# Kernel optimization log

Measured on AMD Instinct MI355X. Metric: run time of the kernel, lower is better.

Reference implementation:

```python
import jax, jax.numpy as jnp
import numpy as np
from jax.ops import segment_sum

N_NODES = 100000
N_EDGES = 3200000
NUM_FEATURES = 256


def setup_inputs() -> dict:
    key = jax.random.key(0)
    ks = jax.random.split(key, 12)
    def lin(k, fan_in, fan_out):
        bound = 1.0 / np.sqrt(fan_in)
        kw, kb = jax.random.split(k)
        W = jax.random.uniform(kw, (fan_in, fan_out), jnp.float32, -bound, bound)
        b = jax.random.uniform(kb, (fan_out,), jnp.float32, -bound, bound)
        return W, b
    x = jax.random.normal(ks[0], (N_NODES, NUM_FEATURES), jnp.float32)
    edge_index = jax.random.randint(ks[1], (2, N_EDGES), 0, N_NODES, jnp.int64 if jax.config.jax_enable_x64 else jnp.int32)
    W1, b1 = lin(ks[2], NUM_FEATURES, 64)
    W2, b2 = lin(ks[3], 64, 32)
    W3, b3 = lin(ks[4], 32, 16)
    Ws02, bs02 = lin(ks[5], NUM_FEATURES, 32)
    Ws03, bs03 = lin(ks[6], NUM_FEATURES, 16)
    Ws13, bs13 = lin(ks[7], 64, 16)
    Wout, bout = lin(ks[8], 16, 1)
    return dict(x=x, edge_index=edge_index, W1=W1, b1=b1, W2=W2, b2=b2,
                W3=W3, b3=b3, Ws02=Ws02, bs02=bs02, Ws03=Ws03, bs03=bs03,
                Ws13=Ws13, bs13=bs13, Wout=Wout, bout=bout)


def _deg_inv_sqrt(edge_index, n_nodes):
    # gcn_norm with self-loops: degree counted at target nodes, +1 for self-loop
    dst = edge_index[1]
    deg = segment_sum(jnp.ones(edge_index.shape[1], jnp.float32), dst, num_segments=n_nodes) + 1.0
    return jnp.where(deg > 0, jax.lax.rsqrt(deg), 0.0)


def _gcn_conv(x, W, b, edge_index, dinv):
    # PyG GCNConv: h = x W; out[i] = sum_{j->i} dinv[j]*dinv[i]*h[j] + dinv[i]^2*h[i] + b
    src, dst = edge_index[0], edge_index[1]
    h = x @ W                                   # [N, out]
    norm = (dinv[src] * dinv[dst])[:, None]     # [E, 1]
    agg = segment_sum(h[src] * norm, dst, num_segments=x.shape[0])
    agg = agg + (dinv * dinv)[:, None] * h      # self-loop term
    return agg + b


def reference(x, edge_index, W1, b1, W2, b2, W3, b3,
              Ws02, bs02, Ws03, bs03, Ws13, bs13, Wout, bout):
    # Dropout in eval mode (identity).
    dinv = _deg_inv_sqrt(edge_index, x.shape[0])
    x1 = jax.nn.relu(_gcn_conv(x, W1, b1, edge_index, dinv))
    x2 = jax.nn.relu(_gcn_conv(x1, W2, b2, edge_index, dinv) + x @ Ws02 + bs02)
    x3 = jax.nn.relu(_gcn_conv(x2, W3, b3, edge_index, dinv)
                     + x @ Ws03 + bs03 + x1 @ Ws13 + bs13)
    return jax.nn.sigmoid(x3 @ Wout + bout)
```

## Files before the change

### kernel.cpp

```cpp
#include <hip/hip_runtime.h>
#include <hip/hip_bf16.h>
#include <math.h>


#define NBUCK_MAX 512
#define P1_CHUNK 8192
#define EPT 32
#define BCAP 9216

typedef __attribute__((ext_vector_type(8))) short bfrag;
typedef __attribute__((ext_vector_type(4))) float f4_t;

__device__ inline float uaf(unsigned u) { return __uint_as_float(u); }
__device__ inline ushort f2bf(float f) {
    __hip_bfloat16 b = __float2bfloat16(f);
    return *reinterpret_cast<ushort*>(&b);
}
__device__ inline bfrag cvt8(const float4 a, const float4 b) {
    union { ushort u[8]; bfrag f; } r;
    r.u[0] = f2bf(a.x); r.u[1] = f2bf(a.y); r.u[2] = f2bf(a.z); r.u[3] = f2bf(a.w);
    r.u[4] = f2bf(b.x); r.u[5] = f2bf(b.y); r.u[6] = f2bf(b.z); r.u[7] = f2bf(b.w);
    return r.f;
}
__device__ inline bfrag ld_bfrag(const ushort* p) {
    const uint4 raw = *reinterpret_cast<const uint4*>(p);
    return *reinterpret_cast<const bfrag*>(&raw);
}


__global__ __launch_bounds__(256) void bucket_hist_kernel(
    const int* __restrict__ dst, int E, int* __restrict__ bucket_count, int nbuckets)
{
    __shared__ int lhist[NBUCK_MAX];
    for (int i = threadIdx.x; i < nbuckets; i += 256) lhist[i] = 0;
    __syncthreads();
    const int stride = gridDim.x * 256;
    for (int e = blockIdx.x * 256 + threadIdx.x; e < E; e += stride)
        atomicAdd(&lhist[dst[e] >> 8], 1);
    __syncthreads();
    for (int i = threadIdx.x; i < nbuckets; i += 256) {
        int c = lhist[i];
        if (c) atomicAdd(&bucket_count[i], c);
    }
}

__global__ __launch_bounds__(512) void bucket_scan_kernel(
    const int* __restrict__ bucket_count, int* __restrict__ bucket_base,
    int* __restrict__ bucket_cursor, int nbuckets)
{
    __shared__ int tmp[512];
    const int tid = threadIdx.x;
    int v = (tid < nbuckets) ? bucket_count[tid] : 0;
    tmp[tid] = v;
    __syncthreads();
    for (int off = 1; off < 512; off <<= 1) {
        int t = (tid >= off) ? tmp[tid - off] : 0;
        __syncthreads();
        tmp[tid] += t;
        __syncthreads();
    }
    if (tid < nbuckets) {
        int base = tmp[tid] - v;
        bucket_base[tid]   = base;
        bucket_cursor[tid] = base;
    }
}

__global__ __launch_bounds__(256) void partition_kernel(
    const int* __restrict__ src, const int* __restrict__ dst, int E,
    int* __restrict__ bucket_cursor, unsigned int* __restrict__ keys, int nbuckets)
{
    __shared__ int hist[NBUCK_MAX];
    __shared__ int lofs[NBUCK_MAX];
    __shared__ int gbase[NBUCK_MAX];
    __shared__ int lcur[NBUCK_MAX];
    __shared__ int ssum[256];
    __shared__ unsigned int stage[P1_CHUNK];
    __shared__ int gidx[P1_CHUNK];

    const int tid = threadIdx.x;
    const int e0  = blockIdx.x * P1_CHUNK;
    const int nE  = min(P1_CHUNK, E - e0);

    for (int i = tid; i < NBUCK_MAX; i += 256) { hist[i] = 0; lcur[i] = 0; }
    __syncthreads();

    int myb[EPT];
    unsigned int mypk[EPT];
#pragma unroll
    for (int j = 0; j < EPT; ++j) {
        const int e = e0 + tid + j * 256;
        if (e < E) {
            const int d = dst[e];
            myb[j]  = d >> 8;
            mypk[j] = ((unsigned int)(d & 255) << 17) | (unsigned int)src[e];
            atomicAdd(&hist[myb[j]], 1);
        } else myb[j] = -1;
    }
    __syncthreads();

    int a0 = (2 * tid     < nbuckets) ? hist[2 * tid]     : 0;
    int a1 = (2 * tid + 1 < nbuckets) ? hist[2 * tid + 1] : 0;
    ssum[tid] = a0 + a1;
    __syncthreads();
    for (int off = 1; off < 256; off <<= 1) {
        int t = (tid >= off) ? ssum[tid - off] : 0;
        __syncthreads();
        ssum[tid] += t;
        __syncthreads();
    }
    const int ex = ssum[tid] - (a0 + a1);
    if (2 * tid     < nbuckets) lofs[2 * tid]     = ex;
    if (2 * tid + 1 < nbuckets) lofs[2 * tid + 1] = ex + a0;
    __syncthreads();

    for (int i = tid; i < nbuckets; i += 256)
        gbase[i] = atomicAdd(&bucket_cursor[i], hist[i]);
    __syncthreads();

#pragma unroll
    for (int j = 0; j < EPT; ++j) {
        if (myb[j] >= 0) {
            const int b = myb[j];
            const int l = lofs[b] + atomicAdd(&lcur[b], 1);
            stage[l] = mypk[j];
            gidx[l]  = gbase[b] - lofs[b] + l;
        }
    }
    __syncthreads();

    for (int i = tid; i < nE; i += 256)
        keys[gidx[i]] = stage[i];
}

__global__ __launch_bounds__(256) void csr_build_kernel(
    const unsigned int* __restrict__ keys, const int* __restrict__ bucket_base,
    const int* __restrict__ bucket_count,
    int* __restrict__ row_off, float* __restrict__ dinv, int* __restrict__ col,
    int N, int E)
{
    __shared__ unsigned int inb[BCAP];
    __shared__ int outv[BCAP];
    __shared__ int hist[256];
    __shared__ int lofs[256];
    __shared__ int ssum[256];

    const int tid  = threadIdx.x;
    const int b    = blockIdx.x;
    const int base = bucket_base[b];
    const int cnt  = min(bucket_count[b], BCAP);
    const int n0   = b << 8;
    const int nn   = min(256, N - n0);

    for (int i = tid; i < cnt; i += 256) inb[i] = keys[base + i];
    hist[tid] = 0;
    __syncthreads();

    for (int i = tid; i < cnt; i += 256)
        atomicAdd(&hist[inb[i] >> 17], 1);
    __syncthreads();

    ssum[tid] = hist[tid];
    __syncthreads();
    for (int off = 1; off < 256; off <<= 1) {
        int t = (tid >= off) ? ssum[tid - off] : 0;
        __syncthreads();
        ssum[tid] += t;
        __syncthreads();
    }
    lofs[tid] = ssum[tid] - hist[tid];

    if (tid < nn) {
        row_off[n0 + tid] = base + lofs[tid];
        dinv[n0 + tid]    = rsqrtf((float)hist[tid] + 1.0f);
    }
    if (b == 0 && tid == 0) row_off[N] = E;
    __syncthreads();

    hist[tid] = 0;
    __syncthreads();

    for (int i = tid; i < cnt; i += 256) {
        const unsigned int k = inb[i];
        const int node = k >> 17;
        const int l = lofs[node] + atomicAdd(&hist[node], 1);
        outv[l] = (int)(k & 0x1FFFF);
    }
    __syncthreads();

    for (int i = tid; i < cnt; i += 256)
        col[base + i] = outv[i];
}


__global__ __launch_bounds__(256) void prep_weights_kernel(
    const float* __restrict__ W1, const float* __restrict__ Ws02,
    const float* __restrict__ Ws03, const float* __restrict__ W2,
    const float* __restrict__ Ws13, const float* __restrict__ W3,
    ushort* __restrict__ Wt0, ushort* __restrict__ Wt1, ushort* __restrict__ Wt2)
{
    int idx = blockIdx.x * 256 + threadIdx.x;
    if (idx < 32768) {
        int f = idx >> 8, k = idx & 255;
        float v = 0.f;
        if (f < 64)       v = W1[k * 64 + f];
        else if (f < 96)  v = Ws02[k * 32 + (f - 64)];
        else if (f < 112) v = Ws03[k * 16 + (f - 96)];
        Wt0[idx] = f2bf(v);
    } else if (idx < 32768 + 3072) {
        int t = idx - 32768;
        int f = t >> 6, k = t & 63;
        float v = (f < 32) ? W2[k * 32 + f] : Ws13[k * 16 + (f - 32)];
        Wt1[t] = f2bf(v);
    } else if (idx < 32768 + 3072 + 512) {
        int t = idx - 32768 - 3072;
        int f = t >> 5, k = t & 31;
        Wt2[t] = f2bf(W3[k * 16 + f]);
    }
}


__global__ __launch_bounds__(256, 4) void gemm_mfma0(
    const float* __restrict__ X, const ushort* __restrict__ Wt0,
    const float* __restrict__ bs02, const float* __restrict__ bs03,
    const float* __restrict__ dinv,
    __hip_bfloat16* __restrict__ g1, float* __restrict__ pre2,
    float* __restrict__ pre3, int N)
{
    const int tid  = threadIdx.x;
    const int lane = tid & 63;
    const int wf   = tid >> 6;
    const int n0   = blockIdx.x * 64;
    const int mrow = lane & 15;
    const int kq   = (lane >> 4) * 8;

    f4_t acc[4][2];
#pragma unroll
    for (int a = 0; a < 4; ++a)
#pragma unroll
        for (int b = 0; b < 2; ++b) acc[a][b] = {0.f, 0.f, 0.f, 0.f};

    const float* xrow[4];
#pragma unroll
    for (int mt = 0; mt < 4; ++mt) {
        int r = n0 + mt * 16 + mrow;
        r = (r < N) ? r : (N - 1);
        xrow[mt] = &X[(size_t)r * 256 + kq];
    }
    const ushort* wrow[2];
#pragma unroll
    for (int ft = 0; ft < 2; ++ft)
        wrow[ft] = &Wt0[(size_t)(wf * 32 + ft * 16 + mrow) * 256 + kq];

#pragma unroll
    for (int p = 0; p < 8; ++p) {
        bfrag bf[2];
#pragma unroll
        for (int ft = 0; ft < 2; ++ft)
            bf[ft] = ld_bfrag(&wrow[ft][p * 32]);
        bfrag af[4];
#pragma unroll
        for (int mt = 0; mt < 4; ++mt) {
            const float4 u0 = *reinterpret_cast<const float4*>(&xrow[mt][p * 32]);
            const float4 u1 = *reinterpret_cast<const float4*>(&xrow[mt][p * 32 + 4]);
            af[mt] = cvt8(u0, u1);
        }
#pragma unroll
        for (int mt = 0; mt < 4; ++mt)
#pragma unroll
            for (int ft = 0; ft < 2; ++ft)
                acc[mt][ft] = __builtin_amdgcn_mfma_f32_16x16x32_bf16(
                    af[mt], bf[ft], acc[mt][ft], 0, 0, 0);
    }

#pragma unroll
    for (int mt = 0; mt < 4; ++mt) {
#pragma unroll
        for (int ft = 0; ft < 2; ++ft) {
            const int fg = wf * 32 + ft * 16 + mrow;
#pragma unroll
            for (int r = 0; r < 4; ++r) {
                const int n = n0 + mt * 16 + (lane >> 4) * 4 + r;
                if (n >= N) continue;
                const float a = acc[mt][ft][r];
                if (fg < 64) {
                    g1[(size_t)n * 64 + fg] = __float2bfloat16(dinv[n] * a);
                } else if (fg < 96) {
                    pre2[(size_t)n * 32 + (fg - 64)] = a + bs02[fg - 64];
                } else if (fg < 112) {
                    pre3[(size_t)n * 16 + (fg - 96)] = a + bs03[fg - 96];
                }
            }
        }
    }
}

__global__ __launch_bounds__(256) void gemm_mfma1(
    const ushort* __restrict__ X1, const ushort* __restrict__ Wt1,
    const float* __restrict__ bs13, const float* __restrict__ dinv,
    __hip_bfloat16* __restrict__ g2, float* __restrict__ pre3, int N)
{
    const int tid  = threadIdx.x;
    const int lane = tid & 63;
    const int wave = tid >> 6;
    const int n0   = blockIdx.x * 128 + wave * 32;
    const int mrow = lane & 15;
    const int kq   = (lane >> 4) * 8;

    f4_t acc[2][3];
#pragma unroll
    for (int a = 0; a < 2; ++a)
#pragma unroll
        for (int b = 0; b < 3; ++b) acc[a][b] = {0.f, 0.f, 0.f, 0.f};

    const ushort* xrow[2];
#pragma unroll
    for (int mt = 0; mt < 2; ++mt) {
        int r = n0 + mt * 16 + mrow;
        r = (r < N) ? r : (N - 1);
        xrow[mt] = &X1[(size_t)r * 64 + kq];
    }
    const ushort* wrow[3];
#pragma unroll
    for (int ft = 0; ft < 3; ++ft)
        wrow[ft] = &Wt1[(size_t)(ft * 16 + mrow) * 64 + kq];

#pragma unroll
    for (int p = 0; p < 2; ++p) {
        bfrag af[2], bf[3];
#pragma unroll
        for (int mt = 0; mt < 2; ++mt) af[mt] = ld_bfrag(&xrow[mt][p * 32]);
#pragma unroll
        for (int ft = 0; ft < 3; ++ft) bf[ft] = ld_bfrag(&wrow[ft][p * 32]);
#pragma unroll
        for (int mt = 0; mt < 2; ++mt)
#pragma unroll
            for (int ft = 0; ft < 3; ++ft)
                acc[mt][ft] = __builtin_amdgcn_mfma_f32_16x16x32_bf16(
                    af[mt], bf[ft], acc[mt][ft], 0, 0, 0);
    }

#pragma unroll
    for (int mt = 0; mt < 2; ++mt) {
#pragma unroll
        for (int ft = 0; ft < 3; ++ft) {
            const int fg = ft * 16 + mrow;
#pragma unroll
            for (int r = 0; r < 4; ++r) {
                const int n = n0 + mt * 16 + (lane >> 4) * 4 + r;
                if (n >= N) continue;
                const float a = acc[mt][ft][r];
                if (fg < 32) {
                    g2[(size_t)n * 32 + fg] = __float2bfloat16(dinv[n] * a);
                } else {
                    pre3[(size_t)n * 16 + (fg - 32)] += a + bs13[fg - 32];
                }
            }
        }
    }
}

__global__ __launch_bounds__(256) void gemm_mfma2(
    const ushort* __restrict__ X2, const ushort* __restrict__ Wt2,
    const float* __restrict__ dinv, __hip_bfloat16* __restrict__ g3, int N)
{
    const int tid  = threadIdx.x;
    const int lane = tid & 63;
    const int wave = tid >> 6;
    const int n0   = blockIdx.x * 128 + wave * 32;
    const int mrow = lane & 15;
    const int kq   = (lane >> 4) * 8;

    f4_t acc[2];
#pragma unroll
    for (int a = 0; a < 2; ++a) acc[a] = {0.f, 0.f, 0.f, 0.f};

    const bfrag bf = ld_bfrag(&Wt2[(size_t)mrow * 32 + kq]);
#pragma unroll
    for (int mt = 0; mt < 2; ++mt) {
        int r = n0 + mt * 16 + mrow;
        r = (r < N) ? r : (N - 1);
        const bfrag af = ld_bfrag(&X2[(size_t)r * 32 + kq]);
        acc[mt] = __builtin_amdgcn_mfma_f32_16x16x32_bf16(af, bf, acc[mt], 0, 0, 0);
    }

#pragma unroll
    for (int mt = 0; mt < 2; ++mt) {
#pragma unroll
        for (int r = 0; r < 4; ++r) {
            const int n = n0 + mt * 16 + (lane >> 4) * 4 + r;
            if (n >= N) continue;
            g3[(size_t)n * 16 + mrow] = __float2bfloat16(dinv[n] * acc[mt][r]);
        }
    }
}


template<int F, int MODE>
__global__ __launch_bounds__(256) void agg_kernel(
    const ushort* __restrict__ g, const float* __restrict__ dinv,
    const int* __restrict__ row_off, const int* __restrict__ col,
    const float* __restrict__ bias, const float* __restrict__ pre,
    const float* __restrict__ Wout, const float* __restrict__ bout,
    void* __restrict__ out, int N)
{
    constexpr int FG  = F / 4;
    constexpr int EPW = 64 / FG;
    constexpr int U   = (F == 64) ? 8 : (F == 32 ? 4 : 2);

    const int lane = threadIdx.x & 63;
    const int wv   = threadIdx.x >> 6;
    const int i    = blockIdx.x * 4 + wv;
    if (i >= N) return;

    const int fg = lane % FG;
    const int eo = lane / FG;
    const int fb = fg * 4;

    float a0 = 0.f, a1 = 0.f, a2 = 0.f, a3 = 0.f;
    const int s = row_off[i], e = row_off[i + 1];
    int p = s + eo;
    for (; p + (U - 1) * EPW < e; p += U * EPW) {
        int js[U];
#pragma unroll
        for (int u = 0; u < U; ++u) js[u] = col[p + u * EPW];
        uint2 w[U];
#pragma unroll
        for (int u = 0; u < U; ++u)
            w[u] = *reinterpret_cast<const uint2*>(&g[(size_t)js[u] * F + fb]);
#pragma unroll
        for (int u = 0; u < U; ++u) {
            a0 += uaf(w[u].x << 16);
            a1 += uaf(w[u].x & 0xffff0000u);
            a2 += uaf(w[u].y << 16);
            a3 += uaf(w[u].y & 0xffff0000u);
        }
    }
    for (; p < e; p += EPW) {
        const uint2 w0 = *reinterpret_cast<const uint2*>(&g[(size_t)col[p] * F + fb]);
        a0 += uaf(w0.x << 16);
        a1 += uaf(w0.x & 0xffff0000u);
        a2 += uaf(w0.y << 16);
        a3 += uaf(w0.y & 0xffff0000u);
    }
#pragma unroll
    for (int off = FG; off < 64; off <<= 1) {
        a0 += __shfl_xor(a0, off);
        a1 += __shfl_xor(a1, off);
        a2 += __shfl_xor(a2, off);
        a3 += __shfl_xor(a3, off);
    }

    const uint2 ws = *reinterpret_cast<const uint2*>(&g[(size_t)i * F + fb]);
    const float di = dinv[i];
    float v0 = di * (a0 + uaf(ws.x << 16))         + bias[fb + 0];
    float v1 = di * (a1 + uaf(ws.x & 0xffff0000u)) + bias[fb + 1];
    float v2 = di * (a2 + uaf(ws.y << 16))         + bias[fb + 2];
    float v3 = di * (a3 + uaf(ws.y & 0xffff0000u)) + bias[fb + 3];
    if (MODE != 0) {
        const float4 pv = *reinterpret_cast<const float4*>(&pre[(size_t)i * F + fb]);
        v0 += pv.x; v1 += pv.y; v2 += pv.z; v3 += pv.w;
    }
    v0 = fmaxf(v0, 0.f); v1 = fmaxf(v1, 0.f);
    v2 = fmaxf(v2, 0.f); v3 = fmaxf(v3, 0.f);

    if (MODE != 2) {
        if (lane < FG) {
            uint2 o;
            o.x = (unsigned)f2bf(v0) | ((unsigned)f2bf(v1) << 16);
            o.y = (unsigned)f2bf(v2) | ((unsigned)f2bf(v3) << 16);
            *reinterpret_cast<uint2*>(&((ushort*)out)[(size_t)i * F + fb]) = o;
        }
    } else {
        float t = v0 * Wout[fb] + v1 * Wout[fb + 1] +
                  v2 * Wout[fb + 2] + v3 * Wout[fb + 3];
        t += __shfl_xor(t, 1);
        t += __shfl_xor(t, 2);
        if (lane == 0)
            ((float*)out)[i] = 1.0f / (1.0f + expf(-(t + bout[0])));
    }
}


extern "C" void kernel_launch(void* const* d_in, const int* in_sizes, int n_in,
                              void* d_out, int out_size, void* d_ws, size_t ws_size,
                              hipStream_t stream)
{
    const float* x    = (const float*)d_in[0];
    const int*   edge = (const int*)d_in[1];
    const float* W1   = (const float*)d_in[2];
    const float* b1   = (const float*)d_in[3];
    const float* W2   = (const float*)d_in[4];
    const float* b2   = (const float*)d_in[5];
    const float* W3   = (const float*)d_in[6];
    const float* b3   = (const float*)d_in[7];
    const float* Ws02 = (const float*)d_in[8];
    const float* bs02 = (const float*)d_in[9];
    const float* Ws03 = (const float*)d_in[10];
    const float* bs03 = (const float*)d_in[11];
    const float* Ws13 = (const float*)d_in[12];
    const float* bs13 = (const float*)d_in[13];
    const float* Wout = (const float*)d_in[14];
    const float* bout = (const float*)d_in[15];

    const int N = in_sizes[0] / 256;
    const int E = in_sizes[1] / 2;
    const int* srcv = edge;
    const int* dstv = edge + E;
    const int nbuckets = (N + 255) >> 8;

    char* ws = (char*)d_ws;
    size_t off = 0;
    auto alloc = [&](size_t bytes) -> void* {
        void* p = ws + off;
        off += (bytes + 255) & ~(size_t)255;
        return p;
    };
    unsigned int* keys = (unsigned int*)alloc((size_t)E * 4);
    int*   col      = (int*)  alloc((size_t)E * 4);
    int*   bcount   = (int*)  alloc((size_t)NBUCK_MAX * 4);
    int*   bbase    = (int*)  alloc((size_t)NBUCK_MAX * 4);
    int*   bcursor  = (int*)  alloc((size_t)NBUCK_MAX * 4);
    int*   row_off  = (int*)  alloc((size_t)(N + 1) * 4);
    float* dinv     = (float*)alloc((size_t)N * 4);
    ushort* Wt0     = (ushort*)alloc((size_t)128 * 256 * 2);
    ushort* Wt1     = (ushort*)alloc((size_t)48 * 64 * 2);
    ushort* Wt2     = (ushort*)alloc((size_t)16 * 32 * 2);
    ushort* g1      = (ushort*)alloc((size_t)N * 64 * 2);
    ushort* x1      = (ushort*)alloc((size_t)N * 64 * 2);
    ushort* g2      = (ushort*)alloc((size_t)N * 32 * 2);
    ushort* x2      = (ushort*)alloc((size_t)N * 32 * 2);
    ushort* g3      = (ushort*)alloc((size_t)N * 16 * 2);
    float* pre2     = (float*)alloc((size_t)N * 32 * 4);
    float* pre3     = (float*)alloc((size_t)N * 16 * 4);

    prep_weights_kernel<<<142, 256, 0, stream>>>(W1, Ws02, Ws03, W2, Ws13, W3,
                                                 Wt0, Wt1, Wt2);
    hipMemsetAsync(bcount, 0, (size_t)NBUCK_MAX * 4, stream);
    bucket_hist_kernel<<<1024, 256, 0, stream>>>(dstv, E, bcount, nbuckets);
    bucket_scan_kernel<<<1, 512, 0, stream>>>(bcount, bbase, bcursor, nbuckets);
    partition_kernel<<<(E + P1_CHUNK - 1) / P1_CHUNK, 256, 0, stream>>>(
        srcv, dstv, E, bcursor, keys, nbuckets);
    csr_build_kernel<<<nbuckets, 256, 0, stream>>>(
        keys, bbase, bcount, row_off, dinv, col, N, E);

    const int ab = (N + 3) / 4;

    gemm_mfma0<<<(N + 63) / 64, 256, 0, stream>>>(
        x, Wt0, bs02, bs03, dinv, (__hip_bfloat16*)g1, pre2, pre3, N);
    agg_kernel<64, 0><<<ab, 256, 0, stream>>>(g1, dinv, row_off, col,
                                              b1, nullptr, nullptr, nullptr, x1, N);
    gemm_mfma1<<<(N + 127) / 128, 256, 0, stream>>>(
        x1, Wt1, bs13, dinv, (__hip_bfloat16*)g2, pre3, N);
    agg_kernel<32, 1><<<ab, 256, 0, stream>>>(g2, dinv, row_off, col,
                                              b2, pre2, nullptr, nullptr, x2, N);
    gemm_mfma2<<<(N + 127) / 128, 256, 0, stream>>>(
        x2, Wt2, dinv, (__hip_bfloat16*)g3, N);
    agg_kernel<16, 2><<<ab, 256, 0, stream>>>(g3, dinv, row_off, col,
                                              b3, pre3, Wout, bout, d_out, N);
}
```

Measured before the change: 486.3 us.

## Stage X tile in LDS via async global_load_lds and preload weight fragments

The first GEMM kernel now copies the 64x256 fp32 X tile into shared memory with direct global-to-LDS loads, using an XOR swizzle to avoid bank conflicts. All four wavefronts then read their A fragments from LDS instead of each issuing redundant global loads. Weight fragments for all k-steps are preloaded into registers up front. This cuts repeated global traffic for X but uses 64KB of LDS per block and more registers, so occupancy drops (launch bounds lowered to 2 blocks per SM), and the load phase no longer overlaps with compute.

```diff
diff --git a/kernel.cpp b/kernel.cpp
--- a/kernel.cpp
+++ b/kernel.cpp
@@ -220,13 +220,15 @@
 }
 
 
-__global__ __launch_bounds__(256, 4) void gemm_mfma0(
+__global__ __launch_bounds__(256, 2) void gemm_mfma0(
     const float* __restrict__ X, const ushort* __restrict__ Wt0,
     const float* __restrict__ bs02, const float* __restrict__ bs03,
     const float* __restrict__ dinv,
     __hip_bfloat16* __restrict__ g1, float* __restrict__ pre2,
     float* __restrict__ pre3, int N)
 {
+    __shared__ __align__(16) float Xs[64 * 256];
+
     const int tid  = threadIdx.x;
     const int lane = tid & 63;
     const int wf   = tid >> 6;
@@ -234,35 +236,46 @@
     const int mrow = lane & 15;
     const int kq   = (lane >> 4) * 8;
 
+    bfrag bfr[2][8];
+#pragma unroll
+    for (int ft = 0; ft < 2; ++ft) {
+        const ushort* wr = &Wt0[(size_t)(wf * 32 + ft * 16 + mrow) * 256 + kq];
+#pragma unroll
+        for (int p = 0; p < 8; ++p)
+            bfr[ft][p] = ld_bfrag(&wr[p * 32]);
+    }
+
+    {
+        for (int i = 0; i < 16; ++i) {
+            const int lrow = wf * 16 + i;
+            const int grow = min(n0 + lrow, N - 1);
+            const float* gsrc = X + (size_t)grow * 256 +
+                                (size_t)((lane ^ (lrow & 7)) * 4);
+            __builtin_amdgcn_global_load_lds(
+                (const __attribute__((address_space(1))) unsigned int*)gsrc,
+                (__attribute__((address_space(3))) unsigned int*)&Xs[lrow * 256],
+                16, 0, 0);
+        }
+    }
+    __syncthreads();
+
     f4_t acc[4][2];
 #pragma unroll
     for (int a = 0; a < 4; ++a)
 #pragma unroll
         for (int b = 0; b < 2; ++b) acc[a][b] = {0.f, 0.f, 0.f, 0.f};
 
-    const float* xrow[4];
-#pragma unroll
-    for (int mt = 0; mt < 4; ++mt) {
-        int r = n0 + mt * 16 + mrow;
-        r = (r < N) ? r : (N - 1);
-        xrow[mt] = &X[(size_t)r * 256 + kq];
-    }
-    const ushort* wrow[2];
-#pragma unroll
-    for (int ft = 0; ft < 2; ++ft)
-        wrow[ft] = &Wt0[(size_t)(wf * 32 + ft * 16 + mrow) * 256 + kq];
+    const float4* Xs4 = reinterpret_cast<const float4*>(Xs);
 
 #pragma unroll
     for (int p = 0; p < 8; ++p) {
-        bfrag bf[2];
-#pragma unroll
-        for (int ft = 0; ft < 2; ++ft)
-            bf[ft] = ld_bfrag(&wrow[ft][p * 32]);
         bfrag af[4];
 #pragma unroll
         for (int mt = 0; mt < 4; ++mt) {
-            const float4 u0 = *reinterpret_cast<const float4*>(&xrow[mt][p * 32]);
-            const float4 u1 = *reinterpret_cast<const float4*>(&xrow[mt][p * 32 + 4]);
+            const int r  = mt * 16 + mrow;
+            const int c0 = p * 8 + (lane >> 4) * 2;
+            const float4 u0 = Xs4[r * 64 + (c0 ^ (r & 7))];
+            const float4 u1 = Xs4[r * 64 + ((c0 + 1) ^ (r & 7))];
             af[mt] = cvt8(u0, u1);
         }
 #pragma unroll
@@ -270,7 +283,7 @@
 #pragma unroll
             for (int ft = 0; ft < 2; ++ft)
                 acc[mt][ft] = __builtin_amdgcn_mfma_f32_16x16x32_bf16(
-                    af[mt], bf[ft], acc[mt][ft], 0, 0, 0);
+                    af[mt], bfr[ft][p], acc[mt][ft], 0, 0, 0);
     }
 
 #pragma unroll
```

New measurement: 477.3 us. Within noise of the previous version (-1.8%).
